# Optimization experiments

Measured on AMD Instinct MI355X. Metric: run time of the kernel, lower is better.

The kernel has to match this reference:

```python
import jax, jax.numpy as jnp
import numpy as np

B, T, H, V, L = 256, 64, 1024, 128, 32  # batch, enc len, hidden, vocab, max decode len


def setup_inputs() -> dict:
    key = jax.random.key(0)
    ks = jax.random.split(key, 12)
    s = 1.0 / np.sqrt(H)
    inp = {
        "inputs": jax.random.randint(ks[0], (B, T), 0, V, dtype=jnp.int32),
        "max_len": L,
        # encoder params
        "enc_emb": jax.random.normal(ks[1], (V, H), jnp.float32) * 0.02,
        "enc_W": jax.random.normal(ks[2], (H, 4 * H), jnp.float32) * s,
        "enc_U": jax.random.normal(ks[3], (H, 4 * H), jnp.float32) * s,
        "enc_b": jnp.zeros((4 * H,), jnp.float32),
        # decoder params
        "dec_emb": jax.random.normal(ks[4], (V, H), jnp.float32) * 0.02,
        "dec_W": jax.random.normal(ks[5], (H, 4 * H), jnp.float32) * s,
        "dec_U": jax.random.normal(ks[6], (H, 4 * H), jnp.float32) * s,
        "dec_b": jnp.zeros((4 * H,), jnp.float32),
        # output projection
        "out_W": jax.random.normal(ks[7], (H, V), jnp.float32) * s,
        "out_b": jnp.zeros((V,), jnp.float32),
    }
    return inp


def _lstm_step(h, c, x, W, U, b):
    # Keras gate order: input, forget, cell, output
    z = x @ W + h @ U + b  # [B, 4H]
    i, f, g, o = jnp.split(z, 4, axis=-1)
    i = jax.nn.sigmoid(i)
    f = jax.nn.sigmoid(f)
    g = jnp.tanh(g)
    o = jax.nn.sigmoid(o)
    c2 = f * c + i * g
    h2 = o * jnp.tanh(c2)
    return h2, c2


def reference(inputs, max_len, enc_emb, enc_W, enc_U, enc_b,
              dec_emb, dec_W, dec_U, dec_b, out_W, out_b):
    batch = inputs.shape[0]
    hid = enc_W.shape[0]
    vocab = dec_emb.shape[0]
    delimiter = vocab - 1

    # ---- Encoder (mask_zero=True: masked steps carry state through) ----
    x_emb = enc_emb[inputs]                     # [B, T, H]
    mask = (inputs != 0)                        # [B, T]

    def enc_scan(carry, xs):
        h, c = carry
        x_t, m_t = xs                           # [B,H], [B]
        h2, c2 = _lstm_step(h, c, x_t, enc_W, enc_U, enc_b)
        m = m_t[:, None]
        return (jnp.where(m, h2, h), jnp.where(m, c2, c)), None

    h0 = jnp.zeros((batch, hid), x_emb.dtype)
    c0 = jnp.zeros((batch, hid), x_emb.dtype)
    (h, c), _ = jax.lax.scan(enc_scan, (h0, c0),
                             (x_emb.transpose(1, 0, 2), mask.T))

    # ---- Greedy decoder: embed -> LSTM -> dense -> softmax -> argmax ----
    def dec_scan(carry, _):
        h, c, tok = carry
        x = dec_emb[tok]                        # [B, H]
        m = (tok != 0)[:, None]
        h2, c2 = _lstm_step(h, c, x, dec_W, dec_U, dec_b)
        h2 = jnp.where(m, h2, h)
        c2 = jnp.where(m, c2, c)
        y = jax.nn.softmax(h2 @ out_W + out_b)  # [B, V]
        tok2 = jnp.argmax(y, axis=-1).astype(jnp.int32)
        return (h2, c2, tok2), (y, tok2)

    tok0 = jnp.full((batch,), delimiter, jnp.int32)
    _, (ys, toks) = jax.lax.scan(dec_scan, (h, c, tok0), None, length=max_len)
    outputs = ys.transpose(1, 0, 2)             # [B, max_len, V]
    return outputs, toks
```

## Files before the change

### kernel.cpp

```cpp
#include <hip/hip_runtime.h>
#include <hip/hip_bf16.h>

namespace {
constexpr int BATCH = 256;
constexpr int TENC  = 64;
constexpr int HID   = 1024;
constexpr int VOC   = 128;
constexpr int LDEC  = 32;
constexpr int G4    = 4 * HID;
}

using short8 = __attribute__((ext_vector_type(8))) short;
using f32x4  = __attribute__((ext_vector_type(4))) float;

__device__ __forceinline__ void async16(const void* g, void* l) {
  __builtin_amdgcn_global_load_lds(
      (const __attribute__((address_space(1))) void*)g,
      (__attribute__((address_space(3))) void*)l, 16, 0, 0);
}

__device__ __forceinline__ unsigned short f2bf(float x) {
  unsigned int u = __float_as_uint(x);
  return (unsigned short)((u + 0x7fffu + ((u >> 16) & 1u)) >> 16);
}
__device__ __forceinline__ float bf2f(unsigned short h) {
  return __uint_as_float(((unsigned int)h) << 16);
}

__global__ __launch_bounds__(256) void k_init(float* __restrict__ h0,
                                              float* __restrict__ c,
                                              unsigned int* __restrict__ hpk0,
                                              int* __restrict__ tok) {
  int i = blockIdx.x * 256 + threadIdx.x;
  h0[i] = 0.f;
  c[i]  = 0.f;
  hpk0[i] = 0u;
  if (i < BATCH) tok[i] = VOC - 1;
}

__global__ __launch_bounds__(256) void k_split_u(
    const float* __restrict__ enc_U, const float* __restrict__ dec_U,
    unsigned short* __restrict__ enc_hi, unsigned short* __restrict__ enc_lo,
    unsigned short* __restrict__ dec_hi, unsigned short* __restrict__ dec_lo) {
  const float* U;
  unsigned short *hi_p, *lo_p;
  if (blockIdx.y == 0) { U = enc_U; hi_p = enc_hi; lo_p = enc_lo; }
  else                 { U = dec_U; hi_p = dec_hi; lo_p = dec_lo; }
  const int gid = blockIdx.x * 256 + threadIdx.x;
  const int k = gid >> 12;
  const int n = gid & 4095;
  const float x = U[gid];
  const unsigned short h = f2bf(x);
  const unsigned short l = f2bf(x - bf2f(h));
  const int hidcol = n & 1023, gate = n >> 10;
  const int ct = hidcol >> 5, j = hidcol & 31;
  const int f = gate * 2 + (j >> 4), coln = j & 15;
  const int ks = k >> 5, kq = (k >> 3) & 3, kk = k & 7;
  const int addr = ((((ct * 32 + ks) * 8 + f) * 64 + kq * 16 + coln) << 3) + kk;
  hi_p[addr] = h;
  lo_p[addr] = l;
}

__global__ __launch_bounds__(256) void k_precompute(
    const float* __restrict__ enc_emb, const float* __restrict__ enc_W,
    const float* __restrict__ enc_b,   const float* __restrict__ dec_emb,
    const float* __restrict__ dec_W,   const float* __restrict__ dec_b,
    float* __restrict__ P_enc, float* __restrict__ P_dec) {
  const float* emb; const float* W; const float* bias; float* P;
  if (blockIdx.z == 0) { emb = enc_emb; W = enc_W; bias = enc_b; P = P_enc; }
  else                 { emb = dec_emb; W = dec_W; bias = dec_b; P = P_dec; }

  __shared__ float A_s[2][64][32];
  __shared__ float B_s[2][32][64];

  const int t    = threadIdx.x;
  const int col0 = blockIdx.x * 64;
  const int v0   = blockIdx.y * 64;
  const int tx   = t & 15;
  const int ty   = t >> 4;
  const int a_row = t >> 3, a_kq = (t & 7) * 4;
  const int b_k   = t >> 4, b_cq = (t & 15) * 4;

  float acc[4][4];
#pragma unroll
  for (int r = 0; r < 4; ++r)
#pragma unroll
    for (int j = 0; j < 4; ++j) acc[r][j] = 0.f;

  async16(&emb[(v0 + a_row) * HID + a_kq], &A_s[0][a_row][a_kq]);
  async16(&emb[(v0 + 32 + a_row) * HID + a_kq], &A_s[0][32 + a_row][a_kq]);
  async16(&W[b_k * G4 + col0 + b_cq], &B_s[0][b_k][b_cq]);
  async16(&W[(16 + b_k) * G4 + col0 + b_cq], &B_s[0][16 + b_k][b_cq]);

  for (int tile = 0; tile < 32; ++tile) {
    const int buf = tile & 1;
    __syncthreads();
    if (tile < 31) {
      const int nb = buf ^ 1;
      const int k0 = (tile + 1) * 32;
      async16(&emb[(v0 + a_row) * HID + k0 + a_kq], &A_s[nb][a_row][a_kq]);
      async16(&emb[(v0 + 32 + a_row) * HID + k0 + a_kq],
              &A_s[nb][32 + a_row][a_kq]);
      async16(&W[(k0 + b_k) * G4 + col0 + b_cq], &B_s[nb][b_k][b_cq]);
      async16(&W[(k0 + 16 + b_k) * G4 + col0 + b_cq],
              &B_s[nb][16 + b_k][b_cq]);
    }
#pragma unroll
    for (int k4 = 0; k4 < 32; k4 += 4) {
      float4 av[4];
#pragma unroll
      for (int r = 0; r < 4; ++r)
        av[r] = *(const float4*)&A_s[buf][ty * 4 + r][k4];
#pragma unroll
      for (int q = 0; q < 4; ++q) {
        const float4 b = *(const float4*)&B_s[buf][k4 + q][tx * 4];
#pragma unroll
        for (int r = 0; r < 4; ++r) {
          const float a = ((const float*)&av[r])[q];
          acc[r][0] += a * b.x;
          acc[r][1] += a * b.y;
          acc[r][2] += a * b.z;
          acc[r][3] += a * b.w;
        }
      }
    }
  }

  const float4 b4 = *(const float4*)&bias[col0 + tx * 4];
#pragma unroll
  for (int r = 0; r < 4; ++r) {
    float4 o;
    o.x = acc[r][0] + b4.x;
    o.y = acc[r][1] + b4.y;
    o.z = acc[r][2] + b4.z;
    o.w = acc[r][3] + b4.w;
    *(float4*)&P[(v0 + ty * 4 + r) * G4 + col0 + tx * 4] = o;
  }
}

__global__ __launch_bounds__(256) void k_cell(
    const float* __restrict__ h_in, float* __restrict__ h_out,
    float* __restrict__ c,
    const unsigned short* __restrict__ Upk_hi,
    const unsigned short* __restrict__ Upk_lo,
    const unsigned short* __restrict__ hpk_in,
    unsigned short* __restrict__ hpk_out,
    const float* __restrict__ P, const int* __restrict__ tok_idx,
    int tok_stride) {
  const int bx = blockIdx.x;
  const int ct = bx & 31;
  const int rt = bx >> 5;
  const int j0 = ct * 32;
  const int r0 = rt * 32;
  const int t    = threadIdx.x;
  const int lane = t & 63;
  const int g    = t >> 6;

  __shared__ char smem[64 * 1024 + 32 * 132 * 4];
  char* Bs = smem;
  float(*z_s)[132] = (float(*)[132])(smem + 64 * 1024);

  const unsigned short* Upk[2] = {Upk_hi, Upk_lo};

#define STAGE(T, buf)                                                        \
  {                                                                          \
    _Pragma("unroll") for (int i = 0; i < 8; ++i) {                          \
      const int cc = t + i * 256;                                            \
      const int lc = cc & 63, ff = (cc >> 6) & 7, k2 = (cc >> 9) & 1,        \
                ss = cc >> 10;                                               \
      const unsigned short* src =                                            \
          Upk[ss] + ((((ct * 32 + (2 * (T) + k2)) * 8 + ff) * 64 + lc) << 3);\
      async16(src, Bs + (buf) * 32768 + cc * 16);                            \
    }                                                                        \
  }

  f32x4 acc[2][2];
#pragma unroll
  for (int m = 0; m < 2; ++m)
#pragma unroll
    for (int n = 0; n < 2; ++n) acc[m][n] = (f32x4){0.f, 0.f, 0.f, 0.f};

  STAGE(0, 0);

  for (int T = 0; T < 16; ++T) {
    const int buf = T & 1;
    __syncthreads();
    if (T < 15) STAGE(T + 1, buf ^ 1);
#pragma unroll
    for (int ks2 = 0; ks2 < 2; ++ks2) {
      const int ks = 2 * T + ks2;
      short8 a[2][2], b[2][2];
#pragma unroll
      for (int m = 0; m < 2; ++m)
#pragma unroll
        for (int s = 0; s < 2; ++s)
          a[m][s] = *(const short8*)(hpk_in +
              ((((s * 32 + ks) * 16 + (rt * 2 + m)) * 64 + lane) << 3));
#pragma unroll
      for (int nf = 0; nf < 2; ++nf)
#pragma unroll
        for (int s = 0; s < 2; ++s)
          b[nf][s] = *(const short8*)(Bs + buf * 32768 +
              ((s * 1024 + ks2 * 512 + (g * 2 + nf) * 64 + lane) << 4));
#pragma unroll
      for (int m = 0; m < 2; ++m)
#pragma unroll
        for (int n = 0; n < 2; ++n) {
          acc[m][n] = __builtin_amdgcn_mfma_f32_16x16x32_bf16(
              a[m][0], b[n][0], acc[m][n], 0, 0, 0);
          acc[m][n] = __builtin_amdgcn_mfma_f32_16x16x32_bf16(
              a[m][0], b[n][1], acc[m][n], 0, 0, 0);
          acc[m][n] = __builtin_amdgcn_mfma_f32_16x16x32_bf16(
              a[m][1], b[n][0], acc[m][n], 0, 0, 0);
          acc[m][n] = __builtin_amdgcn_mfma_f32_16x16x32_bf16(
              a[m][1], b[n][1], acc[m][n], 0, 0, 0);
        }
    }
  }
#undef STAGE

  __syncthreads();
#pragma unroll
  for (int m = 0; m < 2; ++m)
#pragma unroll
    for (int n = 0; n < 2; ++n)
#pragma unroll
      for (int r = 0; r < 4; ++r) {
        const int row = m * 16 + (lane >> 4) * 4 + r;
        const int col = n * 16 + (lane & 15);
        z_s[row][g * 32 + col] = acc[m][n][r];
      }
  __syncthreads();

  const int hc = t & 31;
#pragma unroll
  for (int p = 0; p < 4; ++p) {
    const int row  = (t >> 5) * 4 + p;
    const int grow = r0 + row;
    const int token = tok_idx[grow * tok_stride];
    const float* Px = P + (size_t)token * G4;
    const int col = j0 + hc;
    const float zi = z_s[row][hc]      + Px[col];
    const float zf = z_s[row][32 + hc] + Px[HID + col];
    const float zg = z_s[row][64 + hc] + Px[2 * HID + col];
    const float zo = z_s[row][96 + hc] + Px[3 * HID + col];
    const float ig = 1.f / (1.f + expf(-zi));
    const float fg = 1.f / (1.f + expf(-zf));
    const float gg = tanhf(zg);
    const float og = 1.f / (1.f + expf(-zo));
    const float c_old = c[grow * HID + col];
    const float c2 = fg * c_old + ig * gg;
    const float h2 = og * tanhf(c2);
    float hfin;
    if (token != 0) {
      hfin = h2;
      h_out[grow * HID + col] = h2;
      c[grow * HID + col]     = c2;
    } else {
      hfin = h_in[grow * HID + col];
      h_out[grow * HID + col] = hfin;
    }
    const unsigned short hi = f2bf(hfin);
    const unsigned short lo = f2bf(hfin - bf2f(hi));
    const int kq = hc >> 3, kk = hc & 7;
    const int base =
        ((((ct) * 16 + (grow >> 4)) * 64 + kq * 16 + (grow & 15)) << 3) + kk;
    hpk_out[base] = hi;
    hpk_out[(32 * 16 * 64 << 3) + base] = lo;
  }
}

__global__ __launch_bounds__(128) void k_logits(
    const float* __restrict__ h, const float* __restrict__ out_W,
    const float* __restrict__ out_b, float* __restrict__ out, int t,
    int* __restrict__ tok) {
  const int b0 = blockIdx.x * 2;
  const int v  = threadIdx.x;

  __shared__ float h_s[2][HID];
  __shared__ float red_v[128];
  __shared__ int   red_i[128];

#pragma unroll
  for (int i = 0; i < 4; ++i) {
    int q  = v + i * 128;
    int r  = q >> 8;
    int kq = (q & 255) * 4;
    *(float4*)&h_s[r][kq] = *(const float4*)&h[(b0 + r) * HID + kq];
  }
  __syncthreads();

  float acc[2];
  acc[0] = out_b[v];
  acc[1] = acc[0];
#pragma unroll 8
  for (int k = 0; k < HID; ++k) {
    const float w = out_W[k * VOC + v];
    acc[0] += h_s[0][k] * w;
    acc[1] += h_s[1][k] * w;
  }

  for (int r = 0; r < 2; ++r) {
    const int b = b0 + r;
    red_v[v] = acc[r];
    red_i[v] = v;
    __syncthreads();
    for (int s = 64; s > 0; s >>= 1) {
      if (v < s) {
        const float ov = red_v[v + s];
        const int   oi = red_i[v + s];
        if (ov > red_v[v] || (ov == red_v[v] && oi < red_i[v])) {
          red_v[v] = ov;
          red_i[v] = oi;
        }
      }
      __syncthreads();
    }
    const float mx  = red_v[0];
    const int amax  = red_i[0];
    __syncthreads();
    const float e = expf(acc[r] - mx);
    red_v[v] = e;
    __syncthreads();
    for (int s = 64; s > 0; s >>= 1) {
      if (v < s) red_v[v] += red_v[v + s];
      __syncthreads();
    }
    const float sum = red_v[0];
    out[b * (LDEC * VOC) + t * VOC + v] = e / sum;
    if (v == 0) {
      tok[b] = amax;
      out[BATCH * LDEC * VOC + t * BATCH + b] = (float)amax;
    }
    __syncthreads();
  }
}

extern "C" void kernel_launch(void* const* d_in, const int* in_sizes, int n_in,
                              void* d_out, int out_size, void* d_ws,
                              size_t ws_size, hipStream_t stream) {
  (void)in_sizes; (void)n_in; (void)out_size; (void)ws_size;
  const int*   inputs  = (const int*)d_in[0];
  const float* enc_emb = (const float*)d_in[2];
  const float* enc_W   = (const float*)d_in[3];
  const float* enc_U   = (const float*)d_in[4];
  const float* enc_b   = (const float*)d_in[5];
  const float* dec_emb = (const float*)d_in[6];
  const float* dec_W   = (const float*)d_in[7];
  const float* dec_U   = (const float*)d_in[8];
  const float* dec_b   = (const float*)d_in[9];
  const float* out_W   = (const float*)d_in[10];
  const float* out_b   = (const float*)d_in[11];
  float* out = (float*)d_out;

  float* ws    = (float*)d_ws;
  float* P_enc = ws;
  float* P_dec = P_enc + VOC * G4;
  float* h0    = P_dec + VOC * G4;
  float* h1    = h0 + BATCH * HID;
  float* c     = h1 + BATCH * HID;
  int*   tok   = (int*)(c + BATCH * HID);
  unsigned short* enc_hi = (unsigned short*)(tok + 256);
  unsigned short* enc_lo = enc_hi + (size_t)HID * G4;
  unsigned short* dec_hi = enc_lo + (size_t)HID * G4;
  unsigned short* dec_lo = dec_hi + (size_t)HID * G4;
  unsigned short* hpk0   = dec_lo + (size_t)HID * G4;
  unsigned short* hpk1   = hpk0 + 2 * BATCH * HID;

  k_init<<<(BATCH * HID) / 256, 256, 0, stream>>>(h0, c, (unsigned int*)hpk0,
                                                  tok);

  dim3 sgrid((HID * G4) / 256, 2);
  k_split_u<<<sgrid, 256, 0, stream>>>(enc_U, dec_U, enc_hi, enc_lo, dec_hi,
                                       dec_lo);

  dim3 pgrid(G4 / 64, 2, 2);
  k_precompute<<<pgrid, 256, 0, stream>>>(enc_emb, enc_W, enc_b, dec_emb,
                                          dec_W, dec_b, P_enc, P_dec);

  float* hin = h0;  float* hout = h1;
  unsigned short* pin = hpk0;  unsigned short* pout = hpk1;
  for (int t = 0; t < TENC; ++t) {
    k_cell<<<256, 256, 0, stream>>>(hin, hout, c, enc_hi, enc_lo, pin, pout,
                                    P_enc, inputs + t, TENC);
    float* tf = hin; hin = hout; hout = tf;
    unsigned short* tp = pin; pin = pout; pout = tp;
  }
  for (int s = 0; s < LDEC; ++s) {
    k_cell<<<256, 256, 0, stream>>>(hin, hout, c, dec_hi, dec_lo, pin, pout,
                                    P_dec, tok, 1);
    k_logits<<<BATCH / 2, 128, 0, stream>>>(hout, out_W, out_b, out, s, tok);
    float* tf = hin; hin = hout; hout = tf;
    unsigned short* tp = pin; pin = pout; pout = tp;
  }
}
```

Baseline: 3.690 ms.

## Load U fragments directly to registers with deep prefetch, drop LDS staging

The LSTM cell kernel stops staging the packed recurrent weights through double-buffered LDS via async global-to-LDS copies. Each wave now loads its A and B MFMA fragments straight from global memory into registers, prefetching four k-steps ahead in a rotating buffer, which removes the per-tile __syncthreads and the LDS round-trip. Launch bounds are set to one block per SM to give the larger register footprint room. The weight split kernel is also rewritten so each thread packs eight k values and writes them as one 16-byte store instead of scattered 2-byte writes. The trade-off is higher register pressure and lower occupancy, and the global loads no longer go through a shared tile.

```diff
diff --git a/kernel.cpp b/kernel.cpp
--- a/kernel.cpp
+++ b/kernel.cpp
@@ -47,18 +47,24 @@
   if (blockIdx.y == 0) { U = enc_U; hi_p = enc_hi; lo_p = enc_lo; }
   else                 { U = dec_U; hi_p = dec_hi; lo_p = dec_lo; }
   const int gid = blockIdx.x * 256 + threadIdx.x;
-  const int k = gid >> 12;
-  const int n = gid & 4095;
-  const float x = U[gid];
-  const unsigned short h = f2bf(x);
-  const unsigned short l = f2bf(x - bf2f(h));
-  const int hidcol = n & 1023, gate = n >> 10;
-  const int ct = hidcol >> 5, j = hidcol & 31;
-  const int f = gate * 2 + (j >> 4), coln = j & 15;
-  const int ks = k >> 5, kq = (k >> 3) & 3, kk = k & 7;
-  const int addr = ((((ct * 32 + ks) * 8 + f) * 64 + kq * 16 + coln) << 3) + kk;
-  hi_p[addr] = h;
-  lo_p[addr] = l;
+  const int lanep = gid & 63;
+  const int kq = lanep >> 4, coln = lanep & 15;
+  const int u = gid >> 6;
+  const int f = u & 7;
+  const int v2 = u >> 3;
+  const int ks = v2 & 31, ct = v2 >> 5;
+  const int n = (f >> 1) * HID + ct * 32 + (f & 1) * 16 + coln;
+  const int kbase = ks * 32 + kq * 8;
+
+  unsigned short hv[8], lv[8];
+#pragma unroll
+  for (int kk = 0; kk < 8; ++kk) {
+    const float x = U[(size_t)(kbase + kk) * G4 + n];
+    hv[kk] = f2bf(x);
+    lv[kk] = f2bf(x - bf2f(hv[kk]));
+  }
+  *(short8*)(hi_p + (size_t)gid * 8) = *(short8*)hv;
+  *(short8*)(lo_p + (size_t)gid * 8) = *(short8*)lv;
 }
 
 __global__ __launch_bounds__(256) void k_precompute(
@@ -138,7 +144,7 @@
   }
 }
 
-__global__ __launch_bounds__(256) void k_cell(
+__global__ __launch_bounds__(256, 1) void k_cell(
     const float* __restrict__ h_in, float* __restrict__ h_out,
     float* __restrict__ c,
     const unsigned short* __restrict__ Upk_hi,
@@ -156,70 +162,70 @@
   const int lane = t & 63;
   const int g    = t >> 6;
 
-  __shared__ char smem[64 * 1024 + 32 * 132 * 4];
-  char* Bs = smem;
-  float(*z_s)[132] = (float(*)[132])(smem + 64 * 1024);
-
-  const unsigned short* Upk[2] = {Upk_hi, Upk_lo};
-
-#define STAGE(T, buf)                                                        \
+  __shared__ float z_s[32][132];
+
+  const unsigned short* pa[2][2];
+  const unsigned short* pb[2][2];
+#pragma unroll
+  for (int m = 0; m < 2; ++m)
+#pragma unroll
+    for (int s = 0; s < 2; ++s)
+      pa[m][s] = hpk_in + ((((s * 32) * 16 + (rt * 2 + m)) * 64 + lane) << 3);
+#pragma unroll
+  for (int nf = 0; nf < 2; ++nf) {
+    pb[nf][0] = Upk_hi + (((ct * 32 * 8 + (g * 2 + nf)) * 64 + lane) << 3);
+    pb[nf][1] = Upk_lo + (((ct * 32 * 8 + (g * 2 + nf)) * 64 + lane) << 3);
+  }
+  constexpr int ASTR = 16 * 64 * 8;
+  constexpr int BSTR = 8 * 64 * 8;
+
+  short8 a[4][2][2], b[4][2][2];
+  f32x4 acc[2][2];
+#pragma unroll
+  for (int m = 0; m < 2; ++m)
+#pragma unroll
+    for (int n = 0; n < 2; ++n) acc[m][n] = (f32x4){0.f, 0.f, 0.f, 0.f};
+
+#define LOADT(T, p)                                                          \
   {                                                                          \
-    _Pragma("unroll") for (int i = 0; i < 8; ++i) {                          \
-      const int cc = t + i * 256;                                            \
-      const int lc = cc & 63, ff = (cc >> 6) & 7, k2 = (cc >> 9) & 1,        \
-                ss = cc >> 10;                                               \
-      const unsigned short* src =                                            \
-          Upk[ss] + ((((ct * 32 + (2 * (T) + k2)) * 8 + ff) * 64 + lc) << 3);\
-      async16(src, Bs + (buf) * 32768 + cc * 16);                            \
-    }                                                                        \
-  }
-
-  f32x4 acc[2][2];
-#pragma unroll
-  for (int m = 0; m < 2; ++m)
-#pragma unroll
-    for (int n = 0; n < 2; ++n) acc[m][n] = (f32x4){0.f, 0.f, 0.f, 0.f};
-
-  STAGE(0, 0);
-
-  for (int T = 0; T < 16; ++T) {
-    const int buf = T & 1;
-    __syncthreads();
-    if (T < 15) STAGE(T + 1, buf ^ 1);
-#pragma unroll
-    for (int ks2 = 0; ks2 < 2; ++ks2) {
-      const int ks = 2 * T + ks2;
-      short8 a[2][2], b[2][2];
-#pragma unroll
-      for (int m = 0; m < 2; ++m)
-#pragma unroll
-        for (int s = 0; s < 2; ++s)
-          a[m][s] = *(const short8*)(hpk_in +
-              ((((s * 32 + ks) * 16 + (rt * 2 + m)) * 64 + lane) << 3));
-#pragma unroll
-      for (int nf = 0; nf < 2; ++nf)
-#pragma unroll
-        for (int s = 0; s < 2; ++s)
-          b[nf][s] = *(const short8*)(Bs + buf * 32768 +
-              ((s * 1024 + ks2 * 512 + (g * 2 + nf) * 64 + lane) << 4));
-#pragma unroll
-      for (int m = 0; m < 2; ++m)
-#pragma unroll
-        for (int n = 0; n < 2; ++n) {
-          acc[m][n] = __builtin_amdgcn_mfma_f32_16x16x32_bf16(
-              a[m][0], b[n][0], acc[m][n], 0, 0, 0);
-          acc[m][n] = __builtin_amdgcn_mfma_f32_16x16x32_bf16(
-              a[m][0], b[n][1], acc[m][n], 0, 0, 0);
-          acc[m][n] = __builtin_amdgcn_mfma_f32_16x16x32_bf16(
-              a[m][1], b[n][0], acc[m][n], 0, 0, 0);
-          acc[m][n] = __builtin_amdgcn_mfma_f32_16x16x32_bf16(
-              a[m][1], b[n][1], acc[m][n], 0, 0, 0);
-        }
-    }
-  }
-#undef STAGE
-
-  __syncthreads();
+    _Pragma("unroll") for (int m = 0; m < 2; ++m)                            \
+        _Pragma("unroll") for (int s = 0; s < 2; ++s)                        \
+            a[p][m][s] = *(const short8*)(pa[m][s] + (T) * ASTR);            \
+    _Pragma("unroll") for (int nf = 0; nf < 2; ++nf)                         \
+        _Pragma("unroll") for (int s = 0; s < 2; ++s)                        \
+            b[p][nf][s] = *(const short8*)(pb[nf][s] + (T) * BSTR);          \
+  }
+#define MFMAT(p)                                                             \
+  _Pragma("unroll") for (int m = 0; m < 2; ++m)                              \
+      _Pragma("unroll") for (int n = 0; n < 2; ++n) {                        \
+    acc[m][n] = __builtin_amdgcn_mfma_f32_16x16x32_bf16(                     \
+        a[p][m][0], b[p][n][0], acc[m][n], 0, 0, 0);                         \
+    acc[m][n] = __builtin_amdgcn_mfma_f32_16x16x32_bf16(                     \
+        a[p][m][0], b[p][n][1], acc[m][n], 0, 0, 0);                         \
+    acc[m][n] = __builtin_amdgcn_mfma_f32_16x16x32_bf16(                     \
+        a[p][m][1], b[p][n][0], acc[m][n], 0, 0, 0);                         \
+    acc[m][n] = __builtin_amdgcn_mfma_f32_16x16x32_bf16(                     \
+        a[p][m][1], b[p][n][1], acc[m][n], 0, 0, 0);                         \
+  }
+
+  LOADT(0, 0)
+  LOADT(1, 1)
+  LOADT(2, 2)
+  LOADT(3, 3)
+
+  for (int T = 0; T < 32; T += 4) {
+    MFMAT(0)
+    if (T + 4 < 32) LOADT(T + 4, 0)
+    MFMAT(1)
+    if (T + 5 < 32) LOADT(T + 5, 1)
+    MFMAT(2)
+    if (T + 6 < 32) LOADT(T + 6, 2)
+    MFMAT(3)
+    if (T + 7 < 32) LOADT(T + 7, 3)
+  }
+#undef LOADT
+#undef MFMAT
+
 #pragma unroll
   for (int m = 0; m < 2; ++m)
 #pragma unroll
@@ -370,7 +376,7 @@
   k_init<<<(BATCH * HID) / 256, 256, 0, stream>>>(h0, c, (unsigned int*)hpk0,
                                                   tok);
 
-  dim3 sgrid((HID * G4) / 256, 2);
+  dim3 sgrid((HID * G4) / 8 / 256, 2);
   k_split_u<<<sgrid, 256, 0, stream>>>(enc_U, dec_U, enc_hi, enc_lo, dec_hi,
                                        dec_lo);
 
```

After: 3.121 ms. 15.4% less time.
